# Performance work log

Measured on AMD Instinct MI355X. Metric: run time of the kernel, lower is better.

## Reference

```python
import jax, jax.numpy as jnp
import numpy as np
from jax import lax

B, T = 4096, 1000
INIT_DIM, HID, HH, OUT = 16, 32, 15, 8


def setup_inputs() -> dict:
    key = jax.random.key(0)
    ks = jax.random.split(key, 12)
    s = 0.1
    inp = {
        "times": jnp.arange(T, dtype=jnp.float32),
        "initial": jax.random.normal(ks[0], (B, INIT_DIM), dtype=jnp.float32),
        # initial_linear: initial_dim -> hidden_dim
        "Wi": jax.random.normal(ks[1], (INIT_DIM, HID), dtype=jnp.float32) * s,
        "bi": jnp.zeros((HID,), jnp.float32),
        # func net (num_layers=3): Linear(HID,HH), Tanh, Linear(HH,HH), Tanh, Linear(HH,HH), Tanh, Linear(HH,HID)
        "Wf0": jax.random.normal(ks[2], (HID, HH), dtype=jnp.float32) * s,
        "bf0": jnp.zeros((HH,), jnp.float32),
        "Wf1": jax.random.normal(ks[3], (HH, HH), dtype=jnp.float32) * s,
        "bf1": jnp.zeros((HH,), jnp.float32),
        "Wf2": jax.random.normal(ks[4], (HH, HH), dtype=jnp.float32) * s,
        "bf2": jnp.zeros((HH,), jnp.float32),
        "Wf3": jax.random.normal(ks[5], (HH, HID), dtype=jnp.float32) * s,
        "bf3": jnp.zeros((HID,), jnp.float32),
        # final_linear: hidden_dim -> output_dim
        "Wl": jax.random.normal(ks[6], (HID, OUT), dtype=jnp.float32) * s,
        "bl": jnp.zeros((OUT,), jnp.float32),
    }
    return inp


def _ode_func(h, Wf0, bf0, Wf1, bf1, Wf2, bf2, Wf3, bf3):
    z = jnp.tanh(h @ Wf0 + bf0)
    z = jnp.tanh(z @ Wf1 + bf1)
    z = jnp.tanh(z @ Wf2 + bf2)
    return z @ Wf3 + bf3


def reference(times, initial, Wi, bi, Wf0, bf0, Wf1, bf1, Wf2, bf2, Wf3, bf3, Wl, bl):
    # initial linear: [B, INIT_DIM] -> [B, HID]
    h0 = initial @ Wi + bi
    dts = times[1:] - times[:-1]  # [T-1]

    def step(h, dt):
        hn = h + dt * _ode_func(h, Wf0, bf0, Wf1, bf1, Wf2, bf2, Wf3, bf3)
        return hn, hn

    _, hs = lax.scan(step, h0, dts)          # [T-1, B, HID]
    traj = jnp.concatenate([h0[None], hs], axis=0)  # [T, B, HID]
    traj = jnp.transpose(traj, (1, 0, 2))    # [B, T, HID]
    return traj @ Wl + bl                    # [B, T, OUT]
```

## Files before the change

kernel.cpp:

```cpp
#include <hip/hip_runtime.h>

#ifndef __has_builtin
#define __has_builtin(x) 0
#endif

constexpr int TN   = 1000;
constexpr int BN   = 4096;
constexpr int HID  = 32;
constexpr int HH   = 15;
constexpr int OUTD = 8;

__device__ __forceinline__ float fexp2(float x) {
#if __has_builtin(__builtin_amdgcn_exp2f)
  return __builtin_amdgcn_exp2f(x);
#else
  return exp2f(x);
#endif
}
__device__ __forceinline__ float frcp(float x) {
#if __has_builtin(__builtin_amdgcn_rcpf)
  return __builtin_amdgcn_rcpf(x);
#else
  return 1.0f / x;
#endif
}

template <int K>
__device__ __forceinline__ float rotk(float x) {
  if constexpr (K == 0) {
    return x;
  } else {
    return __int_as_float(
        __builtin_amdgcn_mov_dpp(__float_as_int(x), 0x120 + K, 0xF, 0xF, true));
  }
}

#define FMAC_DPP(acc, src, w, K)                                            \
  asm volatile("v_fmac_f32_dpp %0, %1, %2 row_ror:" #K                      \
               " row_mask:0xf bank_mask:0xf"                                \
               : "+v"(acc) : "v"(src), "v"(w))

#define MUL_DPP(dst, src, w, K)                                             \
  asm volatile("v_mul_f32_dpp %0, %1, %2 row_ror:" #K                       \
               " row_mask:0xf bank_mask:0xf"                                \
               : "=v"(dst) : "v"(src), "v"(w))

#define MUL_DPP_NOP(dst, src, w, K)                                         \
  asm volatile("s_nop 1\n\t"                                                \
               "v_mul_f32_dpp %0, %1, %2 row_ror:" #K                       \
               " row_mask:0xf bank_mask:0xf"                                \
               : "=v"(dst) : "v"(src), "v"(w))

#define PIN(x) asm volatile("" : "+v"(x))

#define REP16(M) M(0) M(1) M(2) M(3) M(4) M(5) M(6) M(7) \
                 M(8) M(9) M(10) M(11) M(12) M(13) M(14) M(15)
#define REP8(M) M(0) M(1) M(2) M(3) M(4) M(5) M(6) M(7)

__global__ __launch_bounds__(256)
__attribute__((amdgpu_waves_per_eu(1, 1)))
void node_kernel(
    const float* __restrict__ times, const float* __restrict__ initial,
    const float* __restrict__ Wi, const float* __restrict__ bi,
    const float* __restrict__ Wf0, const float* __restrict__ bf0,
    const float* __restrict__ Wf1, const float* __restrict__ bf1,
    const float* __restrict__ Wf2, const float* __restrict__ bf2,
    const float* __restrict__ Wf3, const float* __restrict__ bf3,
    const float* __restrict__ Wl, const float* __restrict__ bl,
    float* __restrict__ out) {
  __shared__ float sdt[TN + 2];

  const int tid = blockIdx.x * 256 + threadIdx.x;
  const int row = tid >> 4;
  const int q   = tid & 15;
  const int c   = q & 7;

  for (int i = threadIdx.x; i < TN + 2; i += 256) {
    float d = 0.f;
    if (i < TN - 1) d = times[i + 1] - times[i];
    sdt[i] = d;
  }

  int s1 = __builtin_amdgcn_mov_dpp(q, 0x121, 0xF, 0xF, true);
  const int dir = (s1 == ((q + 1) & 15)) ? 1 : -1;

  const bool qv = (q < HH);

  const float CS = 2.8853900817779268f;

  float fcol[HID];
#pragma unroll
  for (int e = 0; e < HID; ++e) {
    float s = bf3[e];
#pragma unroll
    for (int p = 0; p < HH; ++p) s += Wf3[p * HID + e];
    fcol[e] = s;
  }
  float w0c[HID], wlc[HID];
#pragma unroll
  for (int e = 0; e < HID; ++e) {
    w0c[e] = qv ? Wf0[e * HH + q] : 0.f;
    wlc[e] = Wl[e * OUTD + c];
  }
  float ba = 0.f, boy = 0.f;
#pragma unroll 4
  for (int e = 0; e < HID; ++e) {
    ba  = fmaf(fcol[e], w0c[e], ba);
    boy = fmaf(fcol[e], wlc[e], boy);
  }
  ba *= CS;

  float cs1 = 0.f, cs2 = 0.f;
  if (qv) {
#pragma unroll
    for (int e = 0; e < HH; ++e) {
      cs1 += Wf1[e * HH + q];
      cs2 += Wf2[e * HH + q];
    }
  }
  float b1s = qv ? (bf1[q] + cs1) * CS : 0.f;
  float b2s = qv ? (bf2[q] + cs2) * CS : 0.f;
  PIN(b1s); PIN(b2s);

#define DECLW(k) float w1_##k, w2_##k, ma_##k;
  REP16(DECLW)
#undef DECLW
#define DECLO(k) float wo_##k;
  REP8(DECLO)
#undef DECLO

#define INITW(k)                                                        \
  {                                                                     \
    int p = (q + dir * (k)) & 15;                                       \
    bool pv = (p < HH);                                                 \
    w1_##k = (pv && qv) ? -2.f * CS * Wf1[p * HH + q] : 0.f;            \
    w2_##k = (pv && qv) ? -2.f * CS * Wf2[p * HH + q] : 0.f;            \
    float s_ = 0.f;                                                     \
    if (pv && qv) {                                                     \
      _Pragma("unroll 4") for (int e = 0; e < HID; ++e)                 \
          s_ = fmaf(Wf3[p * HID + e], w0c[e], s_);                      \
    }                                                                   \
    ma_##k = -2.f * CS * s_;                                            \
    PIN(w1_##k); PIN(w2_##k); PIN(ma_##k);                              \
  }
  REP16(INITW)
#undef INITW

#define INITWO(k)                                                       \
  {                                                                     \
    int p = (q + dir * (k)) & 15;                                       \
    float s_ = 0.f;                                                     \
    if (p < HH) {                                                       \
      _Pragma("unroll 4") for (int e = 0; e < HID; ++e)                 \
          s_ = fmaf(Wf3[p * HID + e], wlc[e], s_);                      \
    }                                                                   \
    wo_##k = -2.f * s_;                                                 \
    PIN(wo_##k);                                                        \
  }
  REP8(INITWO)
#undef INITWO

  float h0 = bi[2 * q + 0];
  float h1 = bi[2 * q + 1];
  {
    const float* ini = initial + (size_t)row * 16;
#pragma unroll
    for (int i = 0; i < 16; ++i) {
      float x = ini[i];
      h0 = fmaf(x, Wi[i * HID + 2 * q + 0], h0);
      h1 = fmaf(x, Wi[i * HID + 2 * q + 1], h1);
    }
  }

  float aa = qv ? bf0[q] : 0.f;
#define A0K(k)                                                  \
  {                                                             \
    float a_ = rotk<k>(h0);                                     \
    float b_ = rotk<k>(h1);                                     \
    int p = (q + dir * (k)) & 15;                               \
    if (qv) {                                                   \
      aa = fmaf(a_, Wf0[(2 * p + 0) * HH + q], aa);             \
      aa = fmaf(b_, Wf0[(2 * p + 1) * HH + q], aa);             \
    }                                                           \
  }
  REP16(A0K)
#undef A0K
  float a0 = CS * aa;

  float o = bl[c];
#define O0K(k)                                                  \
  {                                                             \
    float a_ = rotk<k>(h0);                                     \
    float b_ = rotk<k>(h1);                                     \
    int p = (q + dir * (k)) & 15;                               \
    o = fmaf(a_, Wl[(2 * p + 0) * OUTD + c], o);                \
    o = fmaf(b_, Wl[(2 * p + 1) * OUTD + c], o);                \
  }
  REP16(O0K)
#undef O0K

  unsigned obyte = ((unsigned)row * (unsigned)(TN * OUTD) + (unsigned)c) * 4u;
  char* outb = (char*)out;

  __syncthreads();
  float dv = sdt[0];
  float dn = sdt[1];

#pragma unroll 1
  for (int t = 0; t < TN; ++t) {
    float dnn = sdt[t + 2];

    *(float*)(outb + obyte) = o;
    obyte += OUTD * 4;

    float dtv = dv;
    float a0b = fmaf(dtv, ba, a0);
    float ob  = fmaf(dtv, boy, o);

    float r0 = frcp(fexp2(a0) + 1.0f);

    float s_a = fmaf(r0, w1_0, b1s);
    float s_b, s_c, s_d;
    MUL_DPP_NOP(s_b, r0, w1_1, 1);
    MUL_DPP(s_c, r0, w1_2, 2);
    MUL_DPP(s_d, r0, w1_3, 3);
#define L1S(k, acc) FMAC_DPP(acc, r0, w1_##k, k);
    L1S(4, s_a)  L1S(5, s_b)  L1S(6, s_c)  L1S(7, s_d)
    L1S(8, s_a)  L1S(9, s_b)  L1S(10, s_c) L1S(11, s_d)
    L1S(12, s_a) L1S(13, s_b) L1S(14, s_c) L1S(15, s_d)
#undef L1S
    float a1 = (s_a + s_b) + (s_c + s_d);
    float r1 = frcp(fexp2(a1) + 1.0f);

    float u_a = fmaf(r1, w2_0, b2s);
    float u_b, u_c, u_d;
    MUL_DPP_NOP(u_b, r1, w2_1, 1);
    MUL_DPP(u_c, r1, w2_2, 2);
    MUL_DPP(u_d, r1, w2_3, 3);
#define L2S(k, acc) FMAC_DPP(acc, r1, w2_##k, k);
    L2S(4, u_a)  L2S(5, u_b)  L2S(6, u_c)  L2S(7, u_d)
    L2S(8, u_a)  L2S(9, u_b)  L2S(10, u_c) L2S(11, u_d)
    L2S(12, u_a) L2S(13, u_b) L2S(14, u_c) L2S(15, u_d)
#undef L2S
    float a2 = (u_a + u_b) + (u_c + u_d);
    float r2 = frcp(fexp2(a2) + 1.0f);

    float y_a = r2 * ma_0;
    float p_a = r2 * wo_0;
    float y_b, y_c, y_d, p_b;
    MUL_DPP_NOP(y_b, r2, ma_1, 1);
    MUL_DPP(p_b, r2, wo_1, 1);
    MUL_DPP(y_c, r2, ma_2, 2);
    MUL_DPP(y_d, r2, ma_3, 3);
    FMAC_DPP(p_a, r2, wo_2, 2);
    FMAC_DPP(p_b, r2, wo_3, 3);
    FMAC_DPP(y_a, r2, ma_4, 4);
    FMAC_DPP(p_a, r2, wo_4, 4);
    FMAC_DPP(y_b, r2, ma_5, 5);
    FMAC_DPP(p_b, r2, wo_5, 5);
    FMAC_DPP(y_c, r2, ma_6, 6);
    FMAC_DPP(p_a, r2, wo_6, 6);
    FMAC_DPP(y_d, r2, ma_7, 7);
    FMAC_DPP(p_b, r2, wo_7, 7);
    FMAC_DPP(y_a, r2, ma_8, 8);
    FMAC_DPP(y_b, r2, ma_9, 9);
    FMAC_DPP(y_c, r2, ma_10, 10);
    FMAC_DPP(y_d, r2, ma_11, 11);
    FMAC_DPP(y_a, r2, ma_12, 12);
    FMAC_DPP(y_b, r2, ma_13, 13);
    FMAC_DPP(y_c, r2, ma_14, 14);
    FMAC_DPP(y_d, r2, ma_15, 15);

    float ya   = (y_a + y_b) + (y_c + y_d);
    float osum = p_a + p_b;
    float comb = osum + rotk<8>(osum);
    a0 = fmaf(dtv, ya, a0b);
    o  = fmaf(dtv, comb, ob);

    dv = dn;
    dn = dnn;
  }
}

extern "C" void kernel_launch(void* const* d_in, const int* in_sizes, int n_in,
                              void* d_out, int out_size, void* d_ws, size_t ws_size,
                              hipStream_t stream) {
  (void)in_sizes; (void)n_in; (void)d_ws; (void)ws_size; (void)out_size;
  const float* times   = (const float*)d_in[0];
  const float* initial = (const float*)d_in[1];
  const float* Wi  = (const float*)d_in[2];
  const float* bi  = (const float*)d_in[3];
  const float* Wf0 = (const float*)d_in[4];
  const float* bf0 = (const float*)d_in[5];
  const float* Wf1 = (const float*)d_in[6];
  const float* bf1 = (const float*)d_in[7];
  const float* Wf2 = (const float*)d_in[8];
  const float* bf2 = (const float*)d_in[9];
  const float* Wf3 = (const float*)d_in[10];
  const float* bf3 = (const float*)d_in[11];
  const float* Wl  = (const float*)d_in[12];
  const float* bl  = (const float*)d_in[13];

  dim3 grid((BN * 16) / 256);
  dim3 block(256);
  hipLaunchKernelGGL(node_kernel, grid, block, 0, stream,
                     times, initial, Wi, bi, Wf0, bf0, Wf1, bf1,
                     Wf2, bf2, Wf3, bf3, Wl, bl, (float*)d_out);
}
```

Before: 398.0 us.

## Split each row's recurrence across two 16-lane halves with swizzle reduction

Each batch row is now handled by 32 lanes instead of 16. Each half computes 8 of the 16 rotated DPP multiply-accumulates per layer, and the partial sums are combined with a ds_swizzle across the 16-lane halves. The grid doubles and the waves-per-EU hint relaxes to allow two waves. This shortens the serial per-step dependency chain and raises occupancy, at the cost of extra cross-lane swizzle latency, row_ror-8 selects per layer, and redundant lanes doing duplicated bookkeeping and stores.

```diff
diff --git a/kernel.cpp b/kernel.cpp
--- a/kernel.cpp
+++ b/kernel.cpp
@@ -35,6 +35,11 @@
   }
 }
 
+__device__ __forceinline__ float swz16(float x) {
+  return __int_as_float(
+      __builtin_amdgcn_ds_swizzle(__float_as_int(x), 0x401F));
+}
+
 #define FMAC_DPP(acc, src, w, K)                                            \
   asm volatile("v_fmac_f32_dpp %0, %1, %2 row_ror:" #K                      \
                " row_mask:0xf bank_mask:0xf"                                \
@@ -58,7 +63,7 @@
 #define REP8(M) M(0) M(1) M(2) M(3) M(4) M(5) M(6) M(7)
 
 __global__ __launch_bounds__(256)
-__attribute__((amdgpu_waves_per_eu(1, 1)))
+__attribute__((amdgpu_waves_per_eu(2)))
 void node_kernel(
     const float* __restrict__ times, const float* __restrict__ initial,
     const float* __restrict__ Wi, const float* __restrict__ bi,
@@ -70,10 +75,12 @@
     float* __restrict__ out) {
   __shared__ float sdt[TN + 2];
 
-  const int tid = blockIdx.x * 256 + threadIdx.x;
-  const int row = tid >> 4;
-  const int q   = tid & 15;
-  const int c   = q & 7;
+  const int tid  = blockIdx.x * 256 + threadIdx.x;
+  const int l    = threadIdx.x & 63;
+  const int q    = l & 15;
+  const int half = (l >> 4) & 1;
+  const int row  = (tid >> 6) * 2 + (l >> 5);
+  const int c    = q & 7;
 
   for (int i = threadIdx.x; i < TN + 2; i += 256) {
     float d = 0.f;
@@ -120,45 +127,33 @@
   }
   float b1s = qv ? (bf1[q] + cs1) * CS : 0.f;
   float b2s = qv ? (bf2[q] + cs2) * CS : 0.f;
-  PIN(b1s); PIN(b2s);
-
-#define DECLW(k) float w1_##k, w2_##k, ma_##k;
-  REP16(DECLW)
+  float b1h = half ? 0.f : b1s;
+  float b2h = half ? 0.f : b2s;
+  PIN(b1h); PIN(b2h);
+
+#define DECLW(k) float w1_##k, w2_##k, ma_##k, wo_##k;
+  REP8(DECLW)
 #undef DECLW
-#define DECLO(k) float wo_##k;
-  REP8(DECLO)
-#undef DECLO
 
 #define INITW(k)                                                        \
   {                                                                     \
-    int p = (q + dir * (k)) & 15;                                       \
+    int p = (q + dir * ((k) + 8 * half)) & 15;                          \
     bool pv = (p < HH);                                                 \
     w1_##k = (pv && qv) ? -2.f * CS * Wf1[p * HH + q] : 0.f;            \
     w2_##k = (pv && qv) ? -2.f * CS * Wf2[p * HH + q] : 0.f;            \
-    float s_ = 0.f;                                                     \
-    if (pv && qv) {                                                     \
-      _Pragma("unroll 4") for (int e = 0; e < HID; ++e)                 \
-          s_ = fmaf(Wf3[p * HID + e], w0c[e], s_);                      \
+    float sa_ = 0.f, so_ = 0.f;                                         \
+    if (pv) {                                                           \
+      _Pragma("unroll 4") for (int e = 0; e < HID; ++e) {               \
+        sa_ = fmaf(Wf3[p * HID + e], w0c[e], sa_);                      \
+        so_ = fmaf(Wf3[p * HID + e], wlc[e], so_);                      \
+      }                                                                 \
     }                                                                   \
-    ma_##k = -2.f * CS * s_;                                            \
-    PIN(w1_##k); PIN(w2_##k); PIN(ma_##k);                              \
-  }
-  REP16(INITW)
+    ma_##k = -2.f * CS * sa_;              \
+    wo_##k = -2.f * so_;                                                \
+    PIN(w1_##k); PIN(w2_##k); PIN(ma_##k); PIN(wo_##k);                 \
+  }
+  REP8(INITW)
 #undef INITW
-
-#define INITWO(k)                                                       \
-  {                                                                     \
-    int p = (q + dir * (k)) & 15;                                       \
-    float s_ = 0.f;                                                     \
-    if (p < HH) {                                                       \
-      _Pragma("unroll 4") for (int e = 0; e < HID; ++e)                 \
-          s_ = fmaf(Wf3[p * HID + e], wlc[e], s_);                      \
-    }                                                                   \
-    wo_##k = -2.f * s_;                                                 \
-    PIN(wo_##k);                                                        \
-  }
-  REP8(INITWO)
-#undef INITWO
 
   float h0 = bi[2 * q + 0];
   float h1 = bi[2 * q + 1];
@@ -218,64 +213,52 @@
     float ob  = fmaf(dtv, boy, o);
 
     float r0 = frcp(fexp2(a0) + 1.0f);
-
-    float s_a = fmaf(r0, w1_0, b1s);
-    float s_b, s_c, s_d;
-    MUL_DPP_NOP(s_b, r0, w1_1, 1);
-    MUL_DPP(s_c, r0, w1_2, 2);
-    MUL_DPP(s_d, r0, w1_3, 3);
-#define L1S(k, acc) FMAC_DPP(acc, r0, w1_##k, k);
-    L1S(4, s_a)  L1S(5, s_b)  L1S(6, s_c)  L1S(7, s_d)
-    L1S(8, s_a)  L1S(9, s_b)  L1S(10, s_c) L1S(11, s_d)
-    L1S(12, s_a) L1S(13, s_b) L1S(14, s_c) L1S(15, s_d)
-#undef L1S
-    float a1 = (s_a + s_b) + (s_c + s_d);
+    float r0s = rotk<8>(r0);
+    float w0 = half ? r0s : r0;
+
+    float s_a = fmaf(w0, w1_0, b1h);
+    float s_b;
+    MUL_DPP_NOP(s_b, w0, w1_1, 1);
+    FMAC_DPP(s_a, w0, w1_2, 2); FMAC_DPP(s_b, w0, w1_3, 3);
+    FMAC_DPP(s_a, w0, w1_4, 4); FMAC_DPP(s_b, w0, w1_5, 5);
+    FMAC_DPP(s_a, w0, w1_6, 6); FMAC_DPP(s_b, w0, w1_7, 7);
+    float sp = s_a + s_b;
+    float a1 = sp + swz16(sp);
     float r1 = frcp(fexp2(a1) + 1.0f);
-
-    float u_a = fmaf(r1, w2_0, b2s);
-    float u_b, u_c, u_d;
-    MUL_DPP_NOP(u_b, r1, w2_1, 1);
-    MUL_DPP(u_c, r1, w2_2, 2);
-    MUL_DPP(u_d, r1, w2_3, 3);
-#define L2S(k, acc) FMAC_DPP(acc, r1, w2_##k, k);
-    L2S(4, u_a)  L2S(5, u_b)  L2S(6, u_c)  L2S(7, u_d)
-    L2S(8, u_a)  L2S(9, u_b)  L2S(10, u_c) L2S(11, u_d)
-    L2S(12, u_a) L2S(13, u_b) L2S(14, u_c) L2S(15, u_d)
-#undef L2S
-    float a2 = (u_a + u_b) + (u_c + u_d);
+    float r1s = rotk<8>(r1);
+    float w1v = half ? r1s : r1;
+
+    float u_a = fmaf(w1v, w2_0, b2h);
+    float u_b;
+    MUL_DPP_NOP(u_b, w1v, w2_1, 1);
+    FMAC_DPP(u_a, w1v, w2_2, 2); FMAC_DPP(u_b, w1v, w2_3, 3);
+    FMAC_DPP(u_a, w1v, w2_4, 4); FMAC_DPP(u_b, w1v, w2_5, 5);
+    FMAC_DPP(u_a, w1v, w2_6, 6); FMAC_DPP(u_b, w1v, w2_7, 7);
+    float up = u_a + u_b;
+    float a2 = up + swz16(up);
     float r2 = frcp(fexp2(a2) + 1.0f);
-
-    float y_a = r2 * ma_0;
-    float p_a = r2 * wo_0;
-    float y_b, y_c, y_d, p_b;
-    MUL_DPP_NOP(y_b, r2, ma_1, 1);
-    MUL_DPP(p_b, r2, wo_1, 1);
-    MUL_DPP(y_c, r2, ma_2, 2);
-    MUL_DPP(y_d, r2, ma_3, 3);
-    FMAC_DPP(p_a, r2, wo_2, 2);
-    FMAC_DPP(p_b, r2, wo_3, 3);
-    FMAC_DPP(y_a, r2, ma_4, 4);
-    FMAC_DPP(p_a, r2, wo_4, 4);
-    FMAC_DPP(y_b, r2, ma_5, 5);
-    FMAC_DPP(p_b, r2, wo_5, 5);
-    FMAC_DPP(y_c, r2, ma_6, 6);
-    FMAC_DPP(p_a, r2, wo_6, 6);
-    FMAC_DPP(y_d, r2, ma_7, 7);
-    FMAC_DPP(p_b, r2, wo_7, 7);
-    FMAC_DPP(y_a, r2, ma_8, 8);
-    FMAC_DPP(y_b, r2, ma_9, 9);
-    FMAC_DPP(y_c, r2, ma_10, 10);
-    FMAC_DPP(y_d, r2, ma_11, 11);
-    FMAC_DPP(y_a, r2, ma_12, 12);
-    FMAC_DPP(y_b, r2, ma_13, 13);
-    FMAC_DPP(y_c, r2, ma_14, 14);
-    FMAC_DPP(y_d, r2, ma_15, 15);
-
-    float ya   = (y_a + y_b) + (y_c + y_d);
-    float osum = p_a + p_b;
-    float comb = osum + rotk<8>(osum);
+    float r2s = rotk<8>(r2);
+    float w2v = half ? r2s : r2;
+
+    float y_a = w2v * ma_0;
+    float p_a = w2v * wo_0;
+    float y_b, p_b;
+    MUL_DPP_NOP(y_b, w2v, ma_1, 1);
+    MUL_DPP(p_b, w2v, wo_1, 1);
+    FMAC_DPP(y_a, w2v, ma_2, 2); FMAC_DPP(p_a, w2v, wo_2, 2);
+    FMAC_DPP(y_b, w2v, ma_3, 3); FMAC_DPP(p_b, w2v, wo_3, 3);
+    FMAC_DPP(y_a, w2v, ma_4, 4); FMAC_DPP(p_a, w2v, wo_4, 4);
+    FMAC_DPP(y_b, w2v, ma_5, 5); FMAC_DPP(p_b, w2v, wo_5, 5);
+    FMAC_DPP(y_a, w2v, ma_6, 6); FMAC_DPP(p_a, w2v, wo_6, 6);
+    FMAC_DPP(y_b, w2v, ma_7, 7); FMAC_DPP(p_b, w2v, wo_7, 7);
+
+    float yp  = y_a + y_b;
+    float opp = p_a + p_b;
+    float ya  = yp + swz16(yp);
+    float oc  = opp + swz16(opp);
+
     a0 = fmaf(dtv, ya, a0b);
-    o  = fmaf(dtv, comb, ob);
+    o  = fmaf(dtv, oc, ob);
 
     dv = dn;
     dn = dnn;
@@ -301,7 +284,7 @@
   const float* Wl  = (const float*)d_in[12];
   const float* bl  = (const float*)d_in[13];
 
-  dim3 grid((BN * 16) / 256);
+  dim3 grid((BN * 32) / 256);
   dim3 block(256);
   hipLaunchKernelGGL(node_kernel, grid, block, 0, stream,
                      times, initial, Wi, bi, Wf0, bf0, Wf1, bf1,
```

Result: slower. 491.8 us (+23.6%).
